# Kernel optimization log

Hardware: AMD Instinct MI355X
Metric: run time of the kernel (lower is better)

## Reference

```python
import jax, jax.numpy as jnp
import numpy as np

B = 512          # batch
D = 2048         # num_variables / leaf folds of a balanced binary region graph
K = 32           # num_units (sum/input units per fold)


def setup_inputs() -> dict:
    key = jax.random.key(0)
    k1, k2, k3 = jax.random.split(key, 3)
    # input-layer log-densities per (variable-region, unit): [B, D, K]
    x = jax.random.normal(k1, (B, D, K), dtype=jnp.float32)
    # packed per-fold CP mixing weights for all inner layers: sum_l F_l = D-1 folds
    weights = jax.random.uniform(k2, (D - 1, K, K), dtype=jnp.float32,
                                 minval=0.01, maxval=1.0)  # positive (monotonic)
    # packed fold_idx bookkeeping: layer l gathers children (2f, 2f+1) of prev layer
    idx_list = []
    F = D
    while F > 1:
        F //= 2
        idx_list.append(np.arange(2 * F, dtype=np.int32).reshape(F, 2))
    fold_idx = jnp.asarray(np.concatenate(idx_list, axis=0))  # [D-1, 2]
    # out-mixture logits over the root's K units (num_classes = 1)
    mix_logw = jax.random.normal(k3, (K,), dtype=jnp.float32)
    return {"x": x, "weights": weights, "fold_idx": fold_idx, "mix_logw": mix_logw}


def _log_matmul_exp(a, w):
    # a: [B, F, K] log-values; w: [F, K, Kout] positive weights
    # y_j = log sum_i exp(a_i) * w_ij, computed stably via max-subtraction
    m = jnp.max(a, axis=-1, keepdims=True)
    y = jnp.einsum('bfi,fij->bfj', jnp.exp(a - m), w)
    return jnp.log(y) + m


def reference(x, weights, fold_idx, mix_logw):
    # DAG evaluation: gather via fold_idx, CP layer = log-product of the two
    # gathered children followed by a per-fold log-linear mixture.
    out = x                      # [B, F, K]
    off = 0
    F = x.shape[1]
    while F > 1:                 # static Python loop over log2(D)=11 layers
        F //= 2
        idx = fold_idx[off:off + F]            # [F, 2] child indices (static slice)
        inp = out[:, idx, :]                   # gather -> [B, F, 2, K]
        prod = inp[:, :, 0, :] + inp[:, :, 1, :]   # log-space product node
        out = _log_matmul_exp(prod, weights[off:off + F])  # sum node -> [B, F, K]
        off += F
    # Born real path: outputs = 2 * real(log amp), then MonotonicMixtureLayer
    flat = 2.0 * out[:, 0, :]                  # [B, K]
    logw = jax.nn.log_softmax(mix_logw)        # normalized mixture weights
    return jax.nn.logsumexp(flat + logw[None, :], axis=-1)  # [B]
```

## Files before the change

kernel.cpp:

```cpp
#include <hip/hip_runtime.h>

#define KK 32
#define BATCH 512
#define DD 2048
#define ESTRIDE 36
#define NUNIT (KK * BATCH)

__device__ __forceinline__ float max8(const float p[8]) {
  const float a0 = fmaxf(p[0], p[1]), a1 = fmaxf(p[2], p[3]);
  const float a2 = fmaxf(p[4], p[5]), a3 = fmaxf(p[6], p[7]);
  return fmaxf(fmaxf(a0, a1), fmaxf(a2, a3));
}
__device__ __forceinline__ float max4pm(const float* pm, int lane) {
  return fmaxf(fmaxf(pm[lane], pm[65 + lane]),
               fmaxf(pm[130 + lane], pm[195 + lane]));
}
__device__ __forceinline__ void write_e(float* __restrict__ E, int lane,
                                        int j0, const float p[8], float m) {
  float4* ew = reinterpret_cast<float4*>(E + lane * ESTRIDE + j0);
  ew[0] = make_float4(__expf(p[0] - m), __expf(p[1] - m), __expf(p[2] - m),
                      __expf(p[3] - m));
  ew[1] = make_float4(__expf(p[4] - m), __expf(p[5] - m), __expf(p[6] - m),
                      __expf(p[7] - m));
}
__device__ __forceinline__ void addv8(const float a[8], const float b[8],
                                      float o[8]) {
#pragma unroll
  for (int j = 0; j < 8; ++j) o[j] = a[j] + b[j];
}

#define MAC8(acc, e, w0, w1)                                   \
  acc[0] = fmaf(e, w0.x, acc[0]); acc[1] = fmaf(e, w0.y, acc[1]); \
  acc[2] = fmaf(e, w0.z, acc[2]); acc[3] = fmaf(e, w0.w, acc[3]); \
  acc[4] = fmaf(e, w1.x, acc[4]); acc[5] = fmaf(e, w1.y, acc[5]); \
  acc[6] = fmaf(e, w1.z, acc[6]); acc[7] = fmaf(e, w1.w, acc[7]);

__device__ __forceinline__ void node8_pair(
    const float pa[8], const float pb[8], const float* __restrict__ Wa,
    const float* __restrict__ Wb, float* __restrict__ Ea,
    float* __restrict__ Eb, float* __restrict__ pm, int jg, int lane, int j0,
    float oa[8], float ob[8]) {
  pm[jg * 65 + lane] = max8(pa);
  pm[260 + jg * 65 + lane] = max8(pb);
  __syncthreads();
  const float ma = max4pm(pm, lane);
  const float mb = max4pm(pm + 260, lane);
  write_e(Ea, lane, j0, pa, ma);
  write_e(Eb, lane, j0, pb, mb);
  __syncthreads();

  const float4* era = reinterpret_cast<const float4*>(Ea + lane * ESTRIDE);
  const float4* erb = reinterpret_cast<const float4*>(Eb + lane * ESTRIDE);
  const float4* WLa = reinterpret_cast<const float4*>(Wa) + (j0 >> 2);
  const float4* WLb = reinterpret_cast<const float4*>(Wb) + (j0 >> 2);

  float acca[8], accb[8];
#pragma unroll
  for (int j = 0; j < 8; ++j) { acca[j] = 0.0f; accb[j] = 0.0f; }

#pragma unroll 1
  for (int q = 0; q < 8; ++q) {
    const float4 eva = era[q];
    const float4 evb = erb[q];
    const int i0 = 4 * q;
    {
      const float4 w0 = WLa[(i0 + 0) * 8], w1 = WLa[(i0 + 0) * 8 + 1];
      const float4 v0 = WLb[(i0 + 0) * 8], v1 = WLb[(i0 + 0) * 8 + 1];
      MAC8(acca, eva.x, w0, w1) MAC8(accb, evb.x, v0, v1)
    }
    {
      const float4 w0 = WLa[(i0 + 1) * 8], w1 = WLa[(i0 + 1) * 8 + 1];
      const float4 v0 = WLb[(i0 + 1) * 8], v1 = WLb[(i0 + 1) * 8 + 1];
      MAC8(acca, eva.y, w0, w1) MAC8(accb, evb.y, v0, v1)
    }
    {
      const float4 w0 = WLa[(i0 + 2) * 8], w1 = WLa[(i0 + 2) * 8 + 1];
      const float4 v0 = WLb[(i0 + 2) * 8], v1 = WLb[(i0 + 2) * 8 + 1];
      MAC8(acca, eva.z, w0, w1) MAC8(accb, evb.z, v0, v1)
    }
    {
      const float4 w0 = WLa[(i0 + 3) * 8], w1 = WLa[(i0 + 3) * 8 + 1];
      const float4 v0 = WLb[(i0 + 3) * 8], v1 = WLb[(i0 + 3) * 8 + 1];
      MAC8(acca, eva.w, w0, w1) MAC8(accb, evb.w, v0, v1)
    }
  }
#pragma unroll
  for (int j = 0; j < 8; ++j) {
    oa[j] = __logf(acca[j]) + ma;
    ob[j] = __logf(accb[j]) + mb;
  }
}

__device__ __forceinline__ void node8L(const float p8[8],
                                       const float* __restrict__ Wt,
                                       float* __restrict__ E,
                                       float* __restrict__ pm, int jg,
                                       int lane, int j0, float o8[8]) {
  pm[jg * 65 + lane] = max8(p8);
  __syncthreads();
  const float m = max4pm(pm, lane);
  write_e(E, lane, j0, p8, m);
  __syncthreads();

  const float4* er = reinterpret_cast<const float4*>(E + lane * ESTRIDE);
  const float4* WL = reinterpret_cast<const float4*>(Wt) + (j0 >> 2);
  float acc[8];
#pragma unroll
  for (int j = 0; j < 8; ++j) acc[j] = 0.0f;
#pragma unroll 1
  for (int q = 0; q < 8; ++q) {
    const float4 ev = er[q];
    const int i0 = 4 * q;
    const float4 wa0 = WL[(i0 + 0) * 8], wa1 = WL[(i0 + 0) * 8 + 1];
    const float4 wb0 = WL[(i0 + 1) * 8], wb1 = WL[(i0 + 1) * 8 + 1];
    const float4 wc0 = WL[(i0 + 2) * 8], wc1 = WL[(i0 + 2) * 8 + 1];
    const float4 wd0 = WL[(i0 + 3) * 8], wd1 = WL[(i0 + 3) * 8 + 1];
    MAC8(acc, ev.x, wa0, wa1) MAC8(acc, ev.y, wb0, wb1)
    MAC8(acc, ev.z, wc0, wc1) MAC8(acc, ev.w, wd0, wd1)
  }
#pragma unroll
  for (int j = 0; j < 8; ++j) o8[j] = __logf(acc[j]) + m;
}

__device__ __forceinline__ void pairload_x(const float* __restrict__ xb,
                                           int leaf, int j0, float p[8]) {
  const float4* u = reinterpret_cast<const float4*>(xb + leaf * KK + j0);
  const float4* v = reinterpret_cast<const float4*>(xb + (leaf + 1) * KK + j0);
  const float4 u0 = u[0], u1 = u[1], v0 = v[0], v1 = v[1];
  p[0] = u0.x + v0.x; p[1] = u0.y + v0.y; p[2] = u0.z + v0.z; p[3] = u0.w + v0.w;
  p[4] = u1.x + v1.x; p[5] = u1.y + v1.y; p[6] = u1.z + v1.z; p[7] = u1.w + v1.w;
}

__device__ __forceinline__ void pairload_n(const float* __restrict__ in,
                                           int node, int j0, int b, float p[8]) {
  const float* p0 = in + (size_t)node * NUNIT + (size_t)j0 * BATCH + b;
  const float* p1 = p0 + NUNIT;
#pragma unroll
  for (int k = 0; k < 8; ++k) p[k] = p0[k * BATCH] + p1[k * BATCH];
}

__global__ __launch_bounds__(256, 4) void kern1(const float* __restrict__ x,
                                                const float* __restrict__ W,
                                                float* __restrict__ o) {
  __shared__ __align__(16) float W_lds[7 * KK * KK];
  __shared__ __align__(16) float Ea[64 * ESTRIDE];
  __shared__ __align__(16) float Eb[64 * ESTRIDE];
  __shared__ float pm[2 * 260];
  const int tid = threadIdx.x;
  const int lane = tid & 63;
  const int jg = __builtin_amdgcn_readfirstlane(tid >> 6);
  const int j0 = jg * 8;
  const int b = blockIdx.y * 64 + lane;
  const int chunk = blockIdx.x;
  const int c4 = chunk * 4, c2 = chunk * 2;

  const float4* W4 = reinterpret_cast<const float4*>(W);
  float4* WL4 = reinterpret_cast<float4*>(W_lds);
  WL4[tid]        = W4[(size_t)(c4 + 0) * 256 + tid];
  WL4[256 + tid]  = W4[(size_t)(c4 + 1) * 256 + tid];
  WL4[512 + tid]  = W4[(size_t)(c4 + 2) * 256 + tid];
  WL4[768 + tid]  = W4[(size_t)(c4 + 3) * 256 + tid];
  WL4[1024 + tid] = W4[(size_t)(1024 + c2 + 0) * 256 + tid];
  WL4[1280 + tid] = W4[(size_t)(1024 + c2 + 1) * 256 + tid];
  WL4[1536 + tid] = W4[(size_t)(1536 + chunk) * 256 + tid];

  const float* xb = x + (size_t)b * (DD * KK) + (size_t)chunk * 8 * KK;
  float pA0[8], pB0[8], pA1[8], pB1[8];
  pairload_x(xb, 0, j0, pA0);
  pairload_x(xb, 2, j0, pB0);
  pairload_x(xb, 4, j0, pA1);
  pairload_x(xb, 6, j0, pB1);

  float n0[8], n1[8], n2[8], n3[8], m0[8], m1[8], o8[8], p[8], q[8];

  node8_pair(pA0, pB0, W_lds + 0 * 1024, W_lds + 1 * 1024, Ea, Eb, pm, jg,
             lane, j0, n0, n1);
  node8_pair(pA1, pB1, W_lds + 2 * 1024, W_lds + 3 * 1024, Ea, Eb, pm, jg,
             lane, j0, n2, n3);
  addv8(n0, n1, p);
  addv8(n2, n3, q);
  node8_pair(p, q, W_lds + 4 * 1024, W_lds + 5 * 1024, Ea, Eb, pm, jg, lane,
             j0, m0, m1);
  addv8(m0, m1, p);
  node8L(p, W_lds + 6 * 1024, Ea, pm, jg, lane, j0, o8);

#pragma unroll
  for (int j = 0; j < 8; ++j)
    o[(size_t)chunk * NUNIT + (size_t)(j0 + j) * BATCH + b] = o8[j];
}

__global__ __launch_bounds__(256, 4) void kernT(const float* __restrict__ in,
                                                const float* __restrict__ W,
                                                float* __restrict__ o, int lo,
                                                int hi) {
  __shared__ __align__(16) float W_lds[3 * KK * KK];
  __shared__ __align__(16) float Ea[64 * ESTRIDE];
  __shared__ __align__(16) float Eb[64 * ESTRIDE];
  __shared__ float pm[2 * 260];
  const int tid = threadIdx.x;
  const int lane = tid & 63;
  const int jg = __builtin_amdgcn_readfirstlane(tid >> 6);
  const int j0 = jg * 8;
  const int b = blockIdx.y * 64 + lane;
  const int n = blockIdx.x;

  const float4* W4 = reinterpret_cast<const float4*>(W);
  float4* WL4 = reinterpret_cast<float4*>(W_lds);
  WL4[tid]       = W4[(size_t)(lo + 2 * n + 0) * 256 + tid];
  WL4[256 + tid] = W4[(size_t)(lo + 2 * n + 1) * 256 + tid];
  WL4[512 + tid] = W4[(size_t)(hi + n) * 256 + tid];

  float pa[8], pb[8], r0[8], r1[8], p[8], o8[8];
  pairload_n(in, 4 * n + 0, j0, b, pa);
  pairload_n(in, 4 * n + 2, j0, b, pb);
  node8_pair(pa, pb, W_lds, W_lds + 1024, Ea, Eb, pm, jg, lane, j0, r0, r1);
  addv8(r0, r1, p);
  node8L(p, W_lds + 2048, Ea, pm, jg, lane, j0, o8);

#pragma unroll
  for (int j = 0; j < 8; ++j)
    o[(size_t)n * NUNIT + (size_t)(j0 + j) * BATCH + b] = o8[j];
}

__global__ __launch_bounds__(256, 4) void kernF(const float* __restrict__ in,
                                                const float* __restrict__ W,
                                                const float* __restrict__ mixw,
                                                float* __restrict__ out) {
  __shared__ __align__(16) float W_lds[3 * KK * KK];
  __shared__ __align__(16) float Ea[64 * ESTRIDE];
  __shared__ __align__(16) float Eb[64 * ESTRIDE];
  __shared__ float pm[2 * 260];
  const int tid = threadIdx.x;
  const int lane = tid & 63;
  const int jg = __builtin_amdgcn_readfirstlane(tid >> 6);
  const int j0 = jg * 8;
  const int b = blockIdx.y * 64 + lane;

  const float4* W4 = reinterpret_cast<const float4*>(W);
  float4* WL4 = reinterpret_cast<float4*>(W_lds);
  WL4[tid]       = W4[(size_t)2044 * 256 + tid];
  WL4[256 + tid] = W4[(size_t)2045 * 256 + tid];
  WL4[512 + tid] = W4[(size_t)2046 * 256 + tid];

  float pa[8], pb[8], r0[8], r1[8], p[8], o8[8];
  pairload_n(in, 0, j0, b, pa);
  pairload_n(in, 2, j0, b, pb);
  node8_pair(pa, pb, W_lds, W_lds + 1024, Ea, Eb, pm, jg, lane, j0, r0, r1);
  addv8(r0, r1, p);
  node8L(p, W_lds + 2048, Ea, pm, jg, lane, j0, o8);

  float wv32[KK];
#pragma unroll
  for (int i = 0; i < KK; ++i) wv32[i] = mixw[i];
  float t[KK];
#pragma unroll
  for (int i = 0; i < KK; ++i) t[i] = wv32[i];
#pragma unroll
  for (int s = KK / 2; s >= 1; s >>= 1)
#pragma unroll
    for (int i = 0; i < s; ++i) t[i] = fmaxf(t[i], t[i + s]);
  const float wm = t[0];
  float ws = 0.0f;
#pragma unroll
  for (int i = 0; i < KK; ++i) ws += __expf(wv32[i] - wm);
  const float lsew = __logf(ws) + wm;

  float t8[8];
#pragma unroll
  for (int j = 0; j < 8; ++j) t8[j] = 2.0f * o8[j] + (wv32[j0 + j] - lsew);
  __syncthreads();
  pm[jg * 65 + lane] = max8(t8);
  __syncthreads();
  const float m2 = max4pm(pm, lane);
  float ss = 0.0f;
#pragma unroll
  for (int j = 0; j < 8; ++j) ss += __expf(t8[j] - m2);
  __syncthreads();
  pm[jg * 65 + lane] = ss;
  __syncthreads();
  if (jg == 0) {
    const float s4 = (pm[lane] + pm[65 + lane]) + (pm[130 + lane] + pm[195 + lane]);
    out[b] = __logf(s4) + m2;
  }
}

extern "C" void kernel_launch(void* const* d_in, const int* in_sizes, int n_in,
                              void* d_out, int out_size, void* d_ws,
                              size_t ws_size, hipStream_t stream) {
  const float* x = (const float*)d_in[0];
  const float* W = (const float*)d_in[1];
  const float* mixw = (const float*)d_in[3];
  float* out = (float*)d_out;

  float* A = (float*)d_ws;
  float* Bb = A + (size_t)256 * NUNIT;

  kern1<<<dim3(256, 8), 256, 0, stream>>>(x, W, A);
  kernT<<<dim3(64, 8), 256, 0, stream>>>(A, W, Bb, 1792, 1920);
  kernT<<<dim3(16, 8), 256, 0, stream>>>(Bb, W, A, 1984, 2016);
  kernT<<<dim3(4, 8), 256, 0, stream>>>(A, W, Bb, 2032, 2040);
  kernF<<<dim3(1, 8), 256, 0, stream>>>(Bb, W, mixw, out);
}
```

Measured before the change: 244.0 us.

## Remap threads so each wavefront owns whole batch rows, drop block barriers

Threads are remapped so one 64-lane wavefront covers 32 batch rows across all 32 units, with 16-lane groups each holding 8 units. The per-node max reduction becomes two cross-lane shuffles, so the block-wide __syncthreads and pm scratch array are no longer needed. Both rows in a node pair now share the same weight matrix, which halves weight reads from LDS per FMA. Three-level fused kernels replace the two-level kernT, cutting the launch count from five to four, and next-leaf loads are interleaved with compute. The cost is fewer blocks per grid, a lower occupancy hint (3 instead of 4), and more live registers.

Result: slower. 255.4 us (+4.7%).

```diff
diff --git a/kernel.cpp b/kernel.cpp
--- a/kernel.cpp
+++ b/kernel.cpp
@@ -3,30 +3,37 @@
 #define KK 32
 #define BATCH 512
 #define DD 2048
-#define ESTRIDE 36
 #define NUNIT (KK * BATCH)
+#define EST 36
+#define EWSZ (32 * EST)
 
 __device__ __forceinline__ float max8(const float p[8]) {
   const float a0 = fmaxf(p[0], p[1]), a1 = fmaxf(p[2], p[3]);
   const float a2 = fmaxf(p[4], p[5]), a3 = fmaxf(p[6], p[7]);
   return fmaxf(fmaxf(a0, a1), fmaxf(a2, a3));
 }
-__device__ __forceinline__ float max4pm(const float* pm, int lane) {
-  return fmaxf(fmaxf(pm[lane], pm[65 + lane]),
-               fmaxf(pm[130 + lane], pm[195 + lane]));
-}
-__device__ __forceinline__ void write_e(float* __restrict__ E, int lane,
-                                        int j0, const float p[8], float m) {
-  float4* ew = reinterpret_cast<float4*>(E + lane * ESTRIDE + j0);
+__device__ __forceinline__ float maxall(float v) {
+  v = fmaxf(v, __shfl_xor(v, 16, 64));
+  v = fmaxf(v, __shfl_xor(v, 32, 64));
+  return v;
+}
+__device__ __forceinline__ float sumall(float v) {
+  v += __shfl_xor(v, 16, 64);
+  v += __shfl_xor(v, 32, 64);
+  return v;
+}
+__device__ __forceinline__ void addv8(const float a[8], const float b[8],
+                                      float o[8]) {
+#pragma unroll
+  for (int j = 0; j < 8; ++j) o[j] = a[j] + b[j];
+}
+__device__ __forceinline__ void write_e2(float* __restrict__ Er,
+                                         const float p[8], float m) {
+  float4* ew = reinterpret_cast<float4*>(Er);
   ew[0] = make_float4(__expf(p[0] - m), __expf(p[1] - m), __expf(p[2] - m),
                       __expf(p[3] - m));
   ew[1] = make_float4(__expf(p[4] - m), __expf(p[5] - m), __expf(p[6] - m),
                       __expf(p[7] - m));
-}
-__device__ __forceinline__ void addv8(const float a[8], const float b[8],
-                                      float o[8]) {
-#pragma unroll
-  for (int j = 0; j < 8; ++j) o[j] = a[j] + b[j];
 }
 
 #define MAC8(acc, e, w0, w1)                                   \
@@ -35,24 +42,19 @@
   acc[4] = fmaf(e, w1.x, acc[4]); acc[5] = fmaf(e, w1.y, acc[5]); \
   acc[6] = fmaf(e, w1.z, acc[6]); acc[7] = fmaf(e, w1.w, acc[7]);
 
-__device__ __forceinline__ void node8_pair(
-    const float pa[8], const float pb[8], const float* __restrict__ Wa,
-    const float* __restrict__ Wb, float* __restrict__ Ea,
-    float* __restrict__ Eb, float* __restrict__ pm, int jg, int lane, int j0,
-    float oa[8], float ob[8]) {
-  pm[jg * 65 + lane] = max8(pa);
-  pm[260 + jg * 65 + lane] = max8(pb);
-  __syncthreads();
-  const float ma = max4pm(pm, lane);
-  const float mb = max4pm(pm + 260, lane);
-  write_e(Ea, lane, j0, pa, ma);
-  write_e(Eb, lane, j0, pb, mb);
-  __syncthreads();
-
-  const float4* era = reinterpret_cast<const float4*>(Ea + lane * ESTRIDE);
-  const float4* erb = reinterpret_cast<const float4*>(Eb + lane * ESTRIDE);
-  const float4* WLa = reinterpret_cast<const float4*>(Wa) + (j0 >> 2);
-  const float4* WLb = reinterpret_cast<const float4*>(Wb) + (j0 >> 2);
+__device__ __forceinline__ void node2(const float pa[8], const float pb[8],
+                                      const float* __restrict__ Wt,
+                                      float* __restrict__ Ew, int bi, int jg,
+                                      float oa[8], float ob[8]) {
+  const float ma = maxall(max8(pa));
+  const float mb = maxall(max8(pb));
+  write_e2(Ew + bi * EST + jg * 8, pa, ma);
+  write_e2(Ew + (bi + 16) * EST + jg * 8, pb, mb);
+  asm volatile("s_waitcnt lgkmcnt(0)" ::: "memory");
+
+  const float4* era = reinterpret_cast<const float4*>(Ew + bi * EST);
+  const float4* erb = reinterpret_cast<const float4*>(Ew + (bi + 16) * EST);
+  const float4* WL = reinterpret_cast<const float4*>(Wt) + jg * 2;
 
   float acca[8], accb[8];
 #pragma unroll
@@ -64,24 +66,20 @@
     const float4 evb = erb[q];
     const int i0 = 4 * q;
     {
-      const float4 w0 = WLa[(i0 + 0) * 8], w1 = WLa[(i0 + 0) * 8 + 1];
-      const float4 v0 = WLb[(i0 + 0) * 8], v1 = WLb[(i0 + 0) * 8 + 1];
-      MAC8(acca, eva.x, w0, w1) MAC8(accb, evb.x, v0, v1)
+      const float4 w0 = WL[(i0 + 0) * 8], w1 = WL[(i0 + 0) * 8 + 1];
+      MAC8(acca, eva.x, w0, w1) MAC8(accb, evb.x, w0, w1)
     }
     {
-      const float4 w0 = WLa[(i0 + 1) * 8], w1 = WLa[(i0 + 1) * 8 + 1];
-      const float4 v0 = WLb[(i0 + 1) * 8], v1 = WLb[(i0 + 1) * 8 + 1];
-      MAC8(acca, eva.y, w0, w1) MAC8(accb, evb.y, v0, v1)
+      const float4 w0 = WL[(i0 + 1) * 8], w1 = WL[(i0 + 1) * 8 + 1];
+      MAC8(acca, eva.y, w0, w1) MAC8(accb, evb.y, w0, w1)
     }
     {
-      const float4 w0 = WLa[(i0 + 2) * 8], w1 = WLa[(i0 + 2) * 8 + 1];
-      const float4 v0 = WLb[(i0 + 2) * 8], v1 = WLb[(i0 + 2) * 8 + 1];
-      MAC8(acca, eva.z, w0, w1) MAC8(accb, evb.z, v0, v1)
+      const float4 w0 = WL[(i0 + 2) * 8], w1 = WL[(i0 + 2) * 8 + 1];
+      MAC8(acca, eva.z, w0, w1) MAC8(accb, evb.z, w0, w1)
     }
     {
-      const float4 w0 = WLa[(i0 + 3) * 8], w1 = WLa[(i0 + 3) * 8 + 1];
-      const float4 v0 = WLb[(i0 + 3) * 8], v1 = WLb[(i0 + 3) * 8 + 1];
-      MAC8(acca, eva.w, w0, w1) MAC8(accb, evb.w, v0, v1)
+      const float4 w0 = WL[(i0 + 3) * 8], w1 = WL[(i0 + 3) * 8 + 1];
+      MAC8(acca, eva.w, w0, w1) MAC8(accb, evb.w, w0, w1)
     }
   }
 #pragma unroll
@@ -89,37 +87,6 @@
     oa[j] = __logf(acca[j]) + ma;
     ob[j] = __logf(accb[j]) + mb;
   }
-}
-
-__device__ __forceinline__ void node8L(const float p8[8],
-                                       const float* __restrict__ Wt,
-                                       float* __restrict__ E,
-                                       float* __restrict__ pm, int jg,
-                                       int lane, int j0, float o8[8]) {
-  pm[jg * 65 + lane] = max8(p8);
-  __syncthreads();
-  const float m = max4pm(pm, lane);
-  write_e(E, lane, j0, p8, m);
-  __syncthreads();
-
-  const float4* er = reinterpret_cast<const float4*>(E + lane * ESTRIDE);
-  const float4* WL = reinterpret_cast<const float4*>(Wt) + (j0 >> 2);
-  float acc[8];
-#pragma unroll
-  for (int j = 0; j < 8; ++j) acc[j] = 0.0f;
-#pragma unroll 1
-  for (int q = 0; q < 8; ++q) {
-    const float4 ev = er[q];
-    const int i0 = 4 * q;
-    const float4 wa0 = WL[(i0 + 0) * 8], wa1 = WL[(i0 + 0) * 8 + 1];
-    const float4 wb0 = WL[(i0 + 1) * 8], wb1 = WL[(i0 + 1) * 8 + 1];
-    const float4 wc0 = WL[(i0 + 2) * 8], wc1 = WL[(i0 + 2) * 8 + 1];
-    const float4 wd0 = WL[(i0 + 3) * 8], wd1 = WL[(i0 + 3) * 8 + 1];
-    MAC8(acc, ev.x, wa0, wa1) MAC8(acc, ev.y, wb0, wb1)
-    MAC8(acc, ev.z, wc0, wc1) MAC8(acc, ev.w, wd0, wd1)
-  }
-#pragma unroll
-  for (int j = 0; j < 8; ++j) o8[j] = __logf(acc[j]) + m;
 }
 
 __device__ __forceinline__ void pairload_x(const float* __restrict__ xb,
@@ -139,23 +106,25 @@
   for (int k = 0; k < 8; ++k) p[k] = p0[k * BATCH] + p1[k * BATCH];
 }
 
-__global__ __launch_bounds__(256, 4) void kern1(const float* __restrict__ x,
+__global__ __launch_bounds__(256, 3) void kern1(const float* __restrict__ x,
                                                 const float* __restrict__ W,
                                                 float* __restrict__ o) {
-  __shared__ __align__(16) float W_lds[7 * KK * KK];
-  __shared__ __align__(16) float Ea[64 * ESTRIDE];
-  __shared__ __align__(16) float Eb[64 * ESTRIDE];
-  __shared__ float pm[2 * 260];
+  __shared__ __align__(16) float Wl[7 * 1024];
+  __shared__ __align__(16) float E[4 * EWSZ];
   const int tid = threadIdx.x;
+  const int w = tid >> 6;
   const int lane = tid & 63;
-  const int jg = __builtin_amdgcn_readfirstlane(tid >> 6);
+  const int bi = lane & 15;
+  const int jg = lane >> 4;
   const int j0 = jg * 8;
-  const int b = blockIdx.y * 64 + lane;
   const int chunk = blockIdx.x;
-  const int c4 = chunk * 4, c2 = chunk * 2;
+  const int b0 = blockIdx.y * 128 + w * 32 + bi;
+  const int b1 = b0 + 16;
+  float* Ew = E + w * EWSZ;
 
   const float4* W4 = reinterpret_cast<const float4*>(W);
-  float4* WL4 = reinterpret_cast<float4*>(W_lds);
+  float4* WL4 = reinterpret_cast<float4*>(Wl);
+  const int c4 = 4 * chunk, c2 = 2 * chunk;
   WL4[tid]        = W4[(size_t)(c4 + 0) * 256 + tid];
   WL4[256 + tid]  = W4[(size_t)(c4 + 1) * 256 + tid];
   WL4[512 + tid]  = W4[(size_t)(c4 + 2) * 256 + tid];
@@ -164,123 +133,173 @@
   WL4[1280 + tid] = W4[(size_t)(1024 + c2 + 1) * 256 + tid];
   WL4[1536 + tid] = W4[(size_t)(1536 + chunk) * 256 + tid];
 
-  const float* xb = x + (size_t)b * (DD * KK) + (size_t)chunk * 8 * KK;
-  float pA0[8], pB0[8], pA1[8], pB1[8];
-  pairload_x(xb, 0, j0, pA0);
-  pairload_x(xb, 2, j0, pB0);
-  pairload_x(xb, 4, j0, pA1);
-  pairload_x(xb, 6, j0, pB1);
-
-  float n0[8], n1[8], n2[8], n3[8], m0[8], m1[8], o8[8], p[8], q[8];
-
-  node8_pair(pA0, pB0, W_lds + 0 * 1024, W_lds + 1 * 1024, Ea, Eb, pm, jg,
-             lane, j0, n0, n1);
-  node8_pair(pA1, pB1, W_lds + 2 * 1024, W_lds + 3 * 1024, Ea, Eb, pm, jg,
-             lane, j0, n2, n3);
-  addv8(n0, n1, p);
-  addv8(n2, n3, q);
-  node8_pair(p, q, W_lds + 4 * 1024, W_lds + 5 * 1024, Ea, Eb, pm, jg, lane,
-             j0, m0, m1);
-  addv8(m0, m1, p);
-  node8L(p, W_lds + 6 * 1024, Ea, pm, jg, lane, j0, o8);
-
-#pragma unroll
-  for (int j = 0; j < 8; ++j)
-    o[(size_t)chunk * NUNIT + (size_t)(j0 + j) * BATCH + b] = o8[j];
-}
-
-__global__ __launch_bounds__(256, 4) void kernT(const float* __restrict__ in,
-                                                const float* __restrict__ W,
-                                                float* __restrict__ o, int lo,
-                                                int hi) {
-  __shared__ __align__(16) float W_lds[3 * KK * KK];
-  __shared__ __align__(16) float Ea[64 * ESTRIDE];
-  __shared__ __align__(16) float Eb[64 * ESTRIDE];
-  __shared__ float pm[2 * 260];
+  const float* xa = x + (size_t)b0 * (DD * KK) + (size_t)chunk * 8 * KK;
+  const float* xc = x + (size_t)b1 * (DD * KK) + (size_t)chunk * 8 * KK;
+
+  float pa[8], pb[8], qa[8], qb[8];
+  pairload_x(xa, 0, j0, pa);
+  pairload_x(xc, 0, j0, pb);
+  pairload_x(xa, 2, j0, qa);
+  pairload_x(xc, 2, j0, qb);
+
+  __syncthreads();
+
+  float n0a[8], n0b[8], n1a[8], n1b[8];
+  float s01a[8], s01b[8], s23a[8], s23b[8];
+
+  node2(pa, pb, Wl + 0 * 1024, Ew, bi, jg, n0a, n0b);
+  pairload_x(xa, 4, j0, pa);
+  pairload_x(xc, 4, j0, pb);
+  node2(qa, qb, Wl + 1 * 1024, Ew, bi, jg, n1a, n1b);
+  pairload_x(xa, 6, j0, qa);
+  pairload_x(xc, 6, j0, qb);
+  addv8(n0a, n1a, s01a);
+  addv8(n0b, n1b, s01b);
+  node2(pa, pb, Wl + 2 * 1024, Ew, bi, jg, n0a, n0b);
+  node2(qa, qb, Wl + 3 * 1024, Ew, bi, jg, n1a, n1b);
+  addv8(n0a, n1a, s23a);
+  addv8(n0b, n1b, s23b);
+  node2(s01a, s01b, Wl + 4 * 1024, Ew, bi, jg, n0a, n0b);
+  node2(s23a, s23b, Wl + 5 * 1024, Ew, bi, jg, n1a, n1b);
+  addv8(n0a, n1a, s01a);
+  addv8(n0b, n1b, s01b);
+  node2(s01a, s01b, Wl + 6 * 1024, Ew, bi, jg, n0a, n0b);
+
+#pragma unroll
+  for (int j = 0; j < 8; ++j) {
+    o[(size_t)chunk * NUNIT + (size_t)(j0 + j) * BATCH + b0] = n0a[j];
+    o[(size_t)chunk * NUNIT + (size_t)(j0 + j) * BATCH + b1] = n0b[j];
+  }
+}
+
+__global__ __launch_bounds__(256, 3) void kern3L(const float* __restrict__ in,
+                                                 const float* __restrict__ W,
+                                                 float* __restrict__ o, int b4,
+                                                 int b2, int b1) {
+  __shared__ __align__(16) float Wl[7 * 1024];
+  __shared__ __align__(16) float E[4 * EWSZ];
   const int tid = threadIdx.x;
+  const int w = tid >> 6;
   const int lane = tid & 63;
-  const int jg = __builtin_amdgcn_readfirstlane(tid >> 6);
+  const int bi = lane & 15;
+  const int jg = lane >> 4;
   const int j0 = jg * 8;
-  const int b = blockIdx.y * 64 + lane;
-  const int n = blockIdx.x;
+  const int u = blockIdx.x;
+  const int bb0 = blockIdx.y * 128 + w * 32 + bi;
+  const int bb1 = bb0 + 16;
+  float* Ew = E + w * EWSZ;
 
   const float4* W4 = reinterpret_cast<const float4*>(W);
-  float4* WL4 = reinterpret_cast<float4*>(W_lds);
-  WL4[tid]       = W4[(size_t)(lo + 2 * n + 0) * 256 + tid];
-  WL4[256 + tid] = W4[(size_t)(lo + 2 * n + 1) * 256 + tid];
-  WL4[512 + tid] = W4[(size_t)(hi + n) * 256 + tid];
-
-  float pa[8], pb[8], r0[8], r1[8], p[8], o8[8];
-  pairload_n(in, 4 * n + 0, j0, b, pa);
-  pairload_n(in, 4 * n + 2, j0, b, pb);
-  node8_pair(pa, pb, W_lds, W_lds + 1024, Ea, Eb, pm, jg, lane, j0, r0, r1);
-  addv8(r0, r1, p);
-  node8L(p, W_lds + 2048, Ea, pm, jg, lane, j0, o8);
-
-#pragma unroll
-  for (int j = 0; j < 8; ++j)
-    o[(size_t)n * NUNIT + (size_t)(j0 + j) * BATCH + b] = o8[j];
-}
-
-__global__ __launch_bounds__(256, 4) void kernF(const float* __restrict__ in,
+  float4* WL4 = reinterpret_cast<float4*>(Wl);
+  WL4[tid]        = W4[(size_t)(b4 + 4 * u + 0) * 256 + tid];
+  WL4[256 + tid]  = W4[(size_t)(b4 + 4 * u + 1) * 256 + tid];
+  WL4[512 + tid]  = W4[(size_t)(b4 + 4 * u + 2) * 256 + tid];
+  WL4[768 + tid]  = W4[(size_t)(b4 + 4 * u + 3) * 256 + tid];
+  WL4[1024 + tid] = W4[(size_t)(b2 + 2 * u + 0) * 256 + tid];
+  WL4[1280 + tid] = W4[(size_t)(b2 + 2 * u + 1) * 256 + tid];
+  WL4[1536 + tid] = W4[(size_t)(b1 + u) * 256 + tid];
+
+  float pa[8], pb[8], qa[8], qb[8];
+  pairload_n(in, 8 * u + 0, j0, bb0, pa);
+  pairload_n(in, 8 * u + 0, j0, bb1, pb);
+  pairload_n(in, 8 * u + 2, j0, bb0, qa);
+  pairload_n(in, 8 * u + 2, j0, bb1, qb);
+
+  __syncthreads();
+
+  float n0a[8], n0b[8], n1a[8], n1b[8];
+  float s01a[8], s01b[8], s23a[8], s23b[8];
+
+  node2(pa, pb, Wl + 0 * 1024, Ew, bi, jg, n0a, n0b);
+  pairload_n(in, 8 * u + 4, j0, bb0, pa);
+  pairload_n(in, 8 * u + 4, j0, bb1, pb);
+  node2(qa, qb, Wl + 1 * 1024, Ew, bi, jg, n1a, n1b);
+  pairload_n(in, 8 * u + 6, j0, bb0, qa);
+  pairload_n(in, 8 * u + 6, j0, bb1, qb);
+  addv8(n0a, n1a, s01a);
+  addv8(n0b, n1b, s01b);
+  node2(pa, pb, Wl + 2 * 1024, Ew, bi, jg, n0a, n0b);
+  node2(qa, qb, Wl + 3 * 1024, Ew, bi, jg, n1a, n1b);
+  addv8(n0a, n1a, s23a);
+  addv8(n0b, n1b, s23b);
+  node2(s01a, s01b, Wl + 4 * 1024, Ew, bi, jg, n0a, n0b);
+  node2(s23a, s23b, Wl + 5 * 1024, Ew, bi, jg, n1a, n1b);
+  addv8(n0a, n1a, s01a);
+  addv8(n0b, n1b, s01b);
+  node2(s01a, s01b, Wl + 6 * 1024, Ew, bi, jg, n0a, n0b);
+
+#pragma unroll
+  for (int j = 0; j < 8; ++j) {
+    o[(size_t)u * NUNIT + (size_t)(j0 + j) * BATCH + bb0] = n0a[j];
+    o[(size_t)u * NUNIT + (size_t)(j0 + j) * BATCH + bb1] = n0b[j];
+  }
+}
+
+__global__ __launch_bounds__(256, 3) void kernF(const float* __restrict__ in,
                                                 const float* __restrict__ W,
                                                 const float* __restrict__ mixw,
                                                 float* __restrict__ out) {
-  __shared__ __align__(16) float W_lds[3 * KK * KK];
-  __shared__ __align__(16) float Ea[64 * ESTRIDE];
-  __shared__ __align__(16) float Eb[64 * ESTRIDE];
-  __shared__ float pm[2 * 260];
+  __shared__ __align__(16) float Wl[3 * 1024];
+  __shared__ __align__(16) float E[4 * EWSZ];
   const int tid = threadIdx.x;
+  const int w = tid >> 6;
   const int lane = tid & 63;
-  const int jg = __builtin_amdgcn_readfirstlane(tid >> 6);
+  const int bi = lane & 15;
+  const int jg = lane >> 4;
   const int j0 = jg * 8;
-  const int b = blockIdx.y * 64 + lane;
+  const int bb0 = blockIdx.y * 128 + w * 32 + bi;
+  const int bb1 = bb0 + 16;
+  float* Ew = E + w * EWSZ;
 
   const float4* W4 = reinterpret_cast<const float4*>(W);
-  float4* WL4 = reinterpret_cast<float4*>(W_lds);
+  float4* WL4 = reinterpret_cast<float4*>(Wl);
   WL4[tid]       = W4[(size_t)2044 * 256 + tid];
   WL4[256 + tid] = W4[(size_t)2045 * 256 + tid];
   WL4[512 + tid] = W4[(size_t)2046 * 256 + tid];
 
-  float pa[8], pb[8], r0[8], r1[8], p[8], o8[8];
-  pairload_n(in, 0, j0, b, pa);
-  pairload_n(in, 2, j0, b, pb);
-  node8_pair(pa, pb, W_lds, W_lds + 1024, Ea, Eb, pm, jg, lane, j0, r0, r1);
-  addv8(r0, r1, p);
-  node8L(p, W_lds + 2048, Ea, pm, jg, lane, j0, o8);
-
-  float wv32[KK];
-#pragma unroll
-  for (int i = 0; i < KK; ++i) wv32[i] = mixw[i];
-  float t[KK];
-#pragma unroll
-  for (int i = 0; i < KK; ++i) t[i] = wv32[i];
-#pragma unroll
-  for (int s = KK / 2; s >= 1; s >>= 1)
-#pragma unroll
-    for (int i = 0; i < s; ++i) t[i] = fmaxf(t[i], t[i + s]);
-  const float wm = t[0];
-  float ws = 0.0f;
-#pragma unroll
-  for (int i = 0; i < KK; ++i) ws += __expf(wv32[i] - wm);
-  const float lsew = __logf(ws) + wm;
-
-  float t8[8];
-#pragma unroll
-  for (int j = 0; j < 8; ++j) t8[j] = 2.0f * o8[j] + (wv32[j0 + j] - lsew);
+  float pa[8], pb[8], qa[8], qb[8];
+  pairload_n(in, 0, j0, bb0, pa);
+  pairload_n(in, 0, j0, bb1, pb);
+  pairload_n(in, 2, j0, bb0, qa);
+  pairload_n(in, 2, j0, bb1, qb);
+
   __syncthreads();
-  pm[jg * 65 + lane] = max8(t8);
-  __syncthreads();
-  const float m2 = max4pm(pm, lane);
-  float ss = 0.0f;
-#pragma unroll
-  for (int j = 0; j < 8; ++j) ss += __expf(t8[j] - m2);
-  __syncthreads();
-  pm[jg * 65 + lane] = ss;
-  __syncthreads();
+
+  float n0a[8], n0b[8], n1a[8], n1b[8], sa[8], sb[8];
+  node2(pa, pb, Wl + 0 * 1024, Ew, bi, jg, n0a, n0b);
+  node2(qa, qb, Wl + 1 * 1024, Ew, bi, jg, n1a, n1b);
+  addv8(n0a, n1a, sa);
+  addv8(n0b, n1b, sb);
+  node2(sa, sb, Wl + 2 * 1024, Ew, bi, jg, n0a, n0b);
+
+  float mw[8];
+#pragma unroll
+  for (int j = 0; j < 8; ++j) mw[j] = mixw[j0 + j];
+  const float wm = maxall(max8(mw));
+  float ws8 = 0.0f;
+#pragma unroll
+  for (int j = 0; j < 8; ++j) ws8 += __expf(mw[j] - wm);
+  const float lsew = __logf(sumall(ws8)) + wm;
+
+  float ta[8], tb[8];
+#pragma unroll
+  for (int j = 0; j < 8; ++j) {
+    ta[j] = 2.0f * n0a[j] + (mw[j] - lsew);
+    tb[j] = 2.0f * n0b[j] + (mw[j] - lsew);
+  }
+  const float m2a = maxall(max8(ta));
+  const float m2b = maxall(max8(tb));
+  float ssa = 0.0f, ssb = 0.0f;
+#pragma unroll
+  for (int j = 0; j < 8; ++j) {
+    ssa += __expf(ta[j] - m2a);
+    ssb += __expf(tb[j] - m2b);
+  }
+  ssa = sumall(ssa);
+  ssb = sumall(ssb);
   if (jg == 0) {
-    const float s4 = (pm[lane] + pm[65 + lane]) + (pm[130 + lane] + pm[195 + lane]);
-    out[b] = __logf(s4) + m2;
+    out[bb0] = __logf(ssa) + m2a;
+    out[bb1] = __logf(ssb) + m2b;
   }
 }
 
@@ -294,10 +313,10 @@
 
   float* A = (float*)d_ws;
   float* Bb = A + (size_t)256 * NUNIT;
-
-  kern1<<<dim3(256, 8), 256, 0, stream>>>(x, W, A);
-  kernT<<<dim3(64, 8), 256, 0, stream>>>(A, W, Bb, 1792, 1920);
-  kernT<<<dim3(16, 8), 256, 0, stream>>>(Bb, W, A, 1984, 2016);
-  kernT<<<dim3(4, 8), 256, 0, stream>>>(A, W, Bb, 2032, 2040);
-  kernF<<<dim3(1, 8), 256, 0, stream>>>(Bb, W, mixw, out);
-}
+  float* Cc = Bb + (size_t)32 * NUNIT;
+
+  kern1<<<dim3(256, 4), 256, 0, stream>>>(x, W, A);
+  kern3L<<<dim3(32, 4), 256, 0, stream>>>(A, W, Bb, 1792, 1920, 1984);
+  kern3L<<<dim3(4, 4), 256, 0, stream>>>(Bb, W, Cc, 2016, 2032, 2040);
+  kernF<<<dim3(1, 4), 256, 0, stream>>>(Cc, W, mixw, out);
+}
```
